# Optimization experiments

Hardware: AMD Instinct MI355X
Metric: run time of the kernel (lower is better)

## Reference

```python
import jax, jax.numpy as jnp
import numpy as np

B, N, C, H = 16, 4096, 384, 8
NH = N // H  # per-head patch chunk = 512


def setup_inputs() -> dict:
    key = jax.random.key(0)
    ks = jax.random.split(key, 5)
    s = 1.0 / np.sqrt(N)
    return {
        "x": jax.random.normal(ks[0], (B, N, C), dtype=jnp.float32),
        "wq": jax.random.normal(ks[1], (N, N), dtype=jnp.float32) * s,
        "wkv": jax.random.normal(ks[2], (2 * N, N), dtype=jnp.float32) * s,
        "wproj": jax.random.normal(ks[3], (N, N), dtype=jnp.float32) * s,
        "bproj": jax.random.normal(ks[4], (N,), dtype=jnp.float32) * s,
        "scale": jnp.ones((H, 1, 1), dtype=jnp.float32),
    }


def reference(x, wq, wkv, wproj, bproj, scale):
    # x: [B, N, C] -> token-mixing over patch dim N
    xt = jnp.swapaxes(x, -2, -1)                      # [B, C, N]
    q = jnp.einsum('bcn,mn->bcm', xt, wq)             # [B, C, N]
    kv = jnp.einsum('bcn,mn->bcm', xt, wkv)           # [B, C, 2N]
    q = q.reshape(B, C, H, NH).transpose(0, 2, 1, 3)  # [B, H, C, NH]
    kv = kv.reshape(B, C, 2, H, NH).transpose(2, 0, 3, 1, 4)  # [2, B, H, C, NH]
    k, v = kv[0], kv[1]
    q = q / jnp.linalg.norm(q, axis=-1, keepdims=True)
    k = k / jnp.linalg.norm(k, axis=-1, keepdims=True)
    # channel-reduction kernel trick: [B, H, 1, NH], scaled per head
    kernel_trick = (k * v).sum(axis=-2, keepdims=True) * scale
    o = q * kernel_trick                               # [B, H, C, NH]
    o = o.transpose(0, 2, 1, 3).reshape(B, C, N)       # [B, C, N]
    o = jax.nn.gelu(o, approximate=False)              # torch nn.GELU = exact erf
    o = jnp.einsum('bcn,mn->bcm', o, wproj) + bproj    # proj over patch dim
    return jnp.swapaxes(o, -2, -1)                     # [B, N, C]
```

## Files before the change

### kernel.cpp

```cpp
#include <hip/hip_runtime.h>
#include <hip/hip_bf16.h>
#include <math.h>
#include <stdint.h>

#define B_ 16
#define N_ 4096
#define C_ 384
#define H_ 8
#define NH_ 512

typedef __attribute__((ext_vector_type(8))) short short8;
typedef __attribute__((ext_vector_type(4))) float f32x4;

__device__ __forceinline__ unsigned short f2bf(float x) {
  uint32_t u = __builtin_bit_cast(uint32_t, x);
  uint32_t r = (u + 0x7fffu + ((u >> 16) & 1u)) >> 16;
  return (unsigned short)r;
}
__device__ __forceinline__ float bf2f(unsigned short u) {
  uint32_t v = ((uint32_t)u) << 16;
  return __builtin_bit_cast(float, v);
}

__device__ __forceinline__ void gl2lds16(const void* g, void* l) {
  __builtin_amdgcn_global_load_lds((__attribute__((address_space(1))) void*)g,
                                   (__attribute__((address_space(3))) void*)l,
                                   16, 0, 0);
}

__global__ void cvt_f32_bf16(const float* __restrict__ src,
                             unsigned short* __restrict__ dst, size_t n) {
  size_t i = ((size_t)blockIdx.x * blockDim.x + threadIdx.x) * 8;
  if (i >= n) return;
  float4 a = *(const float4*)(src + i);
  float4 b = *(const float4*)(src + i + 4);
  typedef __attribute__((ext_vector_type(8))) unsigned short u16x8;
  u16x8 o;
  o[0] = f2bf(a.x); o[1] = f2bf(a.y); o[2] = f2bf(a.z); o[3] = f2bf(a.w);
  o[4] = f2bf(b.x); o[5] = f2bf(b.y); o[6] = f2bf(b.z); o[7] = f2bf(b.w);
  *(u16x8*)(dst + i) = o;
}

__global__ __launch_bounds__(256)
void transpose_x(const float* __restrict__ x, unsigned short* __restrict__ xT) {
  __shared__ float tile[64 * 65];
  int b = blockIdx.z;
  int n0 = blockIdx.x * 64;
  int c0 = blockIdx.y * 64;
  int t = threadIdx.x;
  const float* xb = x + (size_t)b * N_ * C_;
  #pragma unroll
  for (int i = 0; i < 16; i++) {
    int r = i * 4 + (t >> 6);
    int cc = t & 63;
    tile[r * 65 + cc] = xb[(size_t)(n0 + r) * C_ + c0 + cc];
  }
  __syncthreads();
  unsigned short* xTb = xT + (size_t)b * C_ * N_;
  #pragma unroll
  for (int i = 0; i < 16; i++) {
    int r = i * 4 + (t >> 6);
    int nn = t & 63;
    xTb[(size_t)(c0 + r) * N_ + n0 + nn] = f2bf(tile[nn * 65 + r]);
  }
}

template <bool BIAS>
__global__ __launch_bounds__(256, 2)
void gemm_bt(const unsigned short* __restrict__ A,
             const unsigned short* __restrict__ Bt,
             void* __restrict__ OutV,
             const float* __restrict__ bias,
             size_t bStride, size_t outStride) {
  __shared__ unsigned short As[128 * 64];
  __shared__ unsigned short Bs[128 * 64];
  const int b  = blockIdx.x;
  const int m0 = blockIdx.y * 128;
  const int c0 = blockIdx.z * 128;
  const int t = threadIdx.x;
  const int lane = t & 63;
  const int w = t >> 6;
  const int wm = (w & 1) * 64;
  const int wn = (w >> 1) * 64;
  const int quad = lane >> 4;
  const int r16  = lane & 15;

  const unsigned short* Bb = Bt + (size_t)b * bStride;

  f32x4 acc[4][4];
  #pragma unroll
  for (int i = 0; i < 4; i++)
    #pragma unroll
    for (int j = 0; j < 4; j++)
      acc[i][j] = (f32x4){0.f, 0.f, 0.f, 0.f};

  const int rs = t >> 3;
  const int q8 = (t & 7) ^ (rs & 7);
  const unsigned short* aSrc = A  + (size_t)(m0 + rs) * 4096 + q8 * 8;
  const unsigned short* bSrc = Bb + (size_t)(c0 + rs) * 4096 + q8 * 8;
  unsigned short* aDst = As + t * 8;
  unsigned short* bDst = Bs + t * 8;

  for (int k0 = 0; k0 < 4096; k0 += 64) {
    #pragma unroll
    for (int p = 0; p < 4; p++) {
      gl2lds16(aSrc + (size_t)p * 32 * 4096 + k0, aDst + p * 2048);
      gl2lds16(bSrc + (size_t)p * 32 * 4096 + k0, bDst + p * 2048);
    }
    __syncthreads();
    #pragma unroll
    for (int kk = 0; kk < 2; kk++) {
      short8 af[4], bfv[4];
      const int cb = kk * 4 + quad;
      #pragma unroll
      for (int i = 0; i < 4; i++) {
        int ra = wm + i * 16 + r16;
        af[i]  = *(const short8*)(As + ra * 64 + ((cb ^ (ra & 7)) * 8));
        int rb = wn + i * 16 + r16;
        bfv[i] = *(const short8*)(Bs + rb * 64 + ((cb ^ (rb & 7)) * 8));
      }
      #pragma unroll
      for (int i = 0; i < 4; i++)
        #pragma unroll
        for (int j = 0; j < 4; j++)
          acc[i][j] = __builtin_amdgcn_mfma_f32_16x16x32_bf16(
              af[i], bfv[j], acc[i][j], 0, 0, 0);
    }
    __syncthreads();
  }

  if (BIAS) {
    float* Out = (float*)OutV + (size_t)b * outStride;
    #pragma unroll
    for (int i = 0; i < 4; i++) {
      #pragma unroll
      for (int v = 0; v < 4; v++) {
        int m = m0 + wm + i * 16 + quad * 4 + v;
        float bi = bias[m];
        #pragma unroll
        for (int j = 0; j < 4; j++) {
          int c = c0 + wn + j * 16 + r16;
          Out[(size_t)m * C_ + c] = acc[i][j][v] + bi;
        }
      }
    }
  } else {
    unsigned short* Out = (unsigned short*)OutV + (size_t)b * outStride;
    #pragma unroll
    for (int i = 0; i < 4; i++) {
      #pragma unroll
      for (int v = 0; v < 4; v++) {
        int m = m0 + wm + i * 16 + quad * 4 + v;
        #pragma unroll
        for (int j = 0; j < 4; j++) {
          int c = c0 + wn + j * 16 + r16;
          Out[(size_t)m * C_ + c] = f2bf(acc[i][j][v]);
        }
      }
    }
  }
}

__global__ __launch_bounds__(512)
void middle(const unsigned short* __restrict__ Y,
            unsigned short* __restrict__ GT,
            const float* __restrict__ scale) {
  const int h = blockIdx.x;
  const int b = blockIdx.y;
  const unsigned short* Yb = Y + (size_t)b * 12288 * C_;
  const unsigned short* Q = Yb + (size_t)(h * NH_) * C_;
  const unsigned short* K = Yb + (size_t)(N_ + h * NH_) * C_;
  const unsigned short* V = Yb + (size_t)(2 * N_ + h * NH_) * C_;
  unsigned short* GTb = GT + (size_t)b * C_ * N_ + h * NH_;

  __shared__ float invq[C_], invk[C_], kt[NH_];
  const int t = threadIdx.x;
  const float sc = scale[h];

  if (t < C_) {
    float sq = 0.f, sk = 0.f;
    for (int n = 0; n < NH_; n++) {
      float qv = bf2f(Q[(size_t)n * C_ + t]);
      float kv = bf2f(K[(size_t)n * C_ + t]);
      sq += qv * qv;
      sk += kv * kv;
    }
    invq[t] = rsqrtf(sq);
    invk[t] = rsqrtf(sk);
  }
  __syncthreads();

  {
    int w = t >> 6, l = t & 63;
    for (int n = w; n < NH_; n += 8) {
      float s = 0.f;
      for (int c = l; c < C_; c += 64)
        s += bf2f(K[(size_t)n * C_ + c]) * invk[c] * bf2f(V[(size_t)n * C_ + c]);
      #pragma unroll
      for (int o = 32; o > 0; o >>= 1) s += __shfl_xor(s, o);
      if (l == 0) kt[n] = s * sc;
    }
  }
  __syncthreads();

  {
    int n = t;
    float ktv = kt[n];
    for (int c = 0; c < C_; c++) {
      float xv = bf2f(Q[(size_t)n * C_ + c]) * invq[c] * ktv;
      float g = 0.5f * xv * (1.0f + erff(xv * 0.70710678118654752f));
      GTb[(size_t)c * N_ + n] = f2bf(g);
    }
  }
}

extern "C" void kernel_launch(void* const* d_in, const int* in_sizes, int n_in,
                              void* d_out, int out_size, void* d_ws, size_t ws_size,
                              hipStream_t stream) {
  const float* x     = (const float*)d_in[0];
  const float* wq    = (const float*)d_in[1];
  const float* wkv   = (const float*)d_in[2];
  const float* wproj = (const float*)d_in[3];
  const float* bproj = (const float*)d_in[4];
  const float* scale = (const float*)d_in[5];

  unsigned short* Wqkv = (unsigned short*)d_ws;
  unsigned short* Wp   = Wqkv + (size_t)12288 * 4096;
  unsigned short* xT   = Wp   + (size_t)4096 * 4096;
  unsigned short* Y    = xT   + (size_t)B_ * C_ * N_;
  unsigned short* GT   = Y    + (size_t)B_ * 12288 * C_;

  const size_t nq  = (size_t)4096 * 4096;
  const size_t nkv = (size_t)8192 * 4096;

  cvt_f32_bf16<<<(int)(nq  / 8 / 256), 256, 0, stream>>>(wq,    Wqkv,      nq);
  cvt_f32_bf16<<<(int)(nkv / 8 / 256), 256, 0, stream>>>(wkv,   Wqkv + nq, nkv);
  cvt_f32_bf16<<<(int)(nq  / 8 / 256), 256, 0, stream>>>(wproj, Wp,        nq);

  transpose_x<<<dim3(64, 6, 16), 256, 0, stream>>>(x, xT);

  gemm_bt<false><<<dim3(16, 96, 3), 256, 0, stream>>>(
      Wqkv, xT, Y, nullptr, (size_t)C_ * N_, (size_t)12288 * C_);

  middle<<<dim3(8, 16), 512, 0, stream>>>(Y, GT, scale);

  gemm_bt<true><<<dim3(16, 32, 3), 256, 0, stream>>>(
      Wp, GT, d_out, bproj, (size_t)C_ * N_, (size_t)N_ * C_);
}
```

Before: 1.391 ms.

## Replace QKV GEMM with batched 256x256 double-buffered pipelined MFMA kernel

Folds the batch dimension into the N dimension of the QKV projection so one large GEMM (12288 x 6144 x 4096) runs with 256x256 tiles, 8 waves, and double-buffered LDS fed by direct global-to-LDS loads. Loads are interleaved between MFMA phases using barriers, setprio and a block-index swizzle for L2 locality. This aims to raise data reuse and hide memory latency compared with the per-batch 128x128 kernel. The Y layout changes to [12288, B*C], so the middle kernel's indexing is updated. In exchange, LDS use and register pressure are higher, and the hand-tuned waitcnt schedule is fragile.

```diff
diff --git a/kernel.cpp b/kernel.cpp
--- a/kernel.cpp
+++ b/kernel.cpp
@@ -1,5 +1,4 @@
 #include <hip/hip_runtime.h>
-#include <hip/hip_bf16.h>
 #include <math.h>
 #include <stdint.h>
 
@@ -8,6 +7,7 @@
 #define C_ 384
 #define H_ 8
 #define NH_ 512
+#define NTOT_ 6144
 
 typedef __attribute__((ext_vector_type(8))) short short8;
 typedef __attribute__((ext_vector_type(4))) float f32x4;
@@ -26,6 +26,17 @@
   __builtin_amdgcn_global_load_lds((__attribute__((address_space(1))) void*)g,
                                    (__attribute__((address_space(3))) void*)l,
                                    16, 0, 0);
+}
+
+__device__ __forceinline__ void phase_mid() {
+  __builtin_amdgcn_s_barrier();
+  asm volatile("s_waitcnt lgkmcnt(0)" ::: "memory");
+  __builtin_amdgcn_sched_barrier(0);
+  __builtin_amdgcn_s_setprio(1);
+}
+__device__ __forceinline__ void phase_end() {
+  __builtin_amdgcn_s_setprio(0);
+  __builtin_amdgcn_s_barrier();
 }
 
 __global__ void cvt_f32_bf16(const float* __restrict__ src,
@@ -63,6 +74,133 @@
     int nn = t & 63;
     xTb[(size_t)(c0 + r) * N_ + n0 + nn] = f2bf(tile[nn * 65 + r]);
   }
+}
+
+__global__ __launch_bounds__(512, 2)
+void gemm256_bt(const unsigned short* __restrict__ A,
+                const unsigned short* __restrict__ Bt,
+                unsigned short* __restrict__ Out) {
+  __shared__ unsigned short As[2][2][128 * 64];
+  __shared__ unsigned short Bs[2][2][128 * 64];
+
+  const int bid = blockIdx.x;
+  const int swz = (bid & 7) * 144 + (bid >> 3);
+  const int mt = swz / 24, nt = swz % 24;
+  const int m0 = mt * 256, n0 = nt * 256;
+
+  const int t = threadIdx.x;
+  const int lane = t & 63;
+  const int w = t >> 6;
+  const int quad = lane >> 4;
+  const int r16 = lane & 15;
+  const int hA = w >> 2;
+  const int hB = (w >> 1) & 1;
+  const int rBb = (w & 1) * 64;
+  const int slot0 = quad ^ (r16 & 7);
+  const int slot1 = slot0 ^ 4;
+
+  f32x4 acc[8][4];
+  #pragma unroll
+  for (int i = 0; i < 8; i++)
+    #pragma unroll
+    for (int j = 0; j < 4; j++)
+      acc[i][j] = (f32x4){0.f, 0.f, 0.f, 0.f};
+
+  short8 af[4][2], bl[2][2], bh[2][2];
+
+  const int rs = t >> 3;
+  const int q8 = (t & 7) ^ (rs & 7);
+  const unsigned short* aS = A  + (size_t)(m0 + rs) * 4096 + q8 * 8;
+  const unsigned short* bS = Bt + (size_t)(n0 + rs) * 4096 + q8 * 8;
+
+  auto stA = [&](int d, int hf, int kt) {
+    const unsigned short* s =
+        aS + (size_t)hf * (128 * 4096) + (size_t)((kt & 63) * 64);
+    unsigned short* dp = &As[d][hf][t * 8];
+    gl2lds16(s, dp);
+    gl2lds16(s + (size_t)64 * 4096, dp + 4096);
+  };
+  auto stB = [&](int d, int hf, int kt) {
+    const unsigned short* s =
+        bS + (size_t)hf * (128 * 4096) + (size_t)((kt & 63) * 64);
+    unsigned short* dp = &Bs[d][hf][t * 8];
+    gl2lds16(s, dp);
+    gl2lds16(s + (size_t)64 * 4096, dp + 4096);
+  };
+  auto ldAh = [&](int d, int ih) {
+    #pragma unroll
+    for (int i = 0; i < 4; i++) {
+      const unsigned short* base = &As[d][hA][(ih * 64 + i * 16 + r16) * 64];
+      af[i][0] = *(const short8*)(base + slot0 * 8);
+      af[i][1] = *(const short8*)(base + slot1 * 8);
+    }
+  };
+  auto ldBh = [&](int d, int jh, short8 (&bfr)[2][2]) {
+    #pragma unroll
+    for (int j = 0; j < 2; j++) {
+      const unsigned short* base =
+          &Bs[d][hB][(rBb + jh * 32 + j * 16 + r16) * 64];
+      bfr[j][0] = *(const short8*)(base + slot0 * 8);
+      bfr[j][1] = *(const short8*)(base + slot1 * 8);
+    }
+  };
+  auto mfma16 = [&](int i0, int j0, short8 (&bfr)[2][2]) {
+    #pragma unroll
+    for (int i = 0; i < 4; i++)
+      #pragma unroll
+      for (int j = 0; j < 2; j++) {
+        acc[i0 + i][j0 + j] = __builtin_amdgcn_mfma_f32_16x16x32_bf16(
+            af[i][0], bfr[j][0], acc[i0 + i][j0 + j], 0, 0, 0);
+        acc[i0 + i][j0 + j] = __builtin_amdgcn_mfma_f32_16x16x32_bf16(
+            af[i][1], bfr[j][1], acc[i0 + i][j0 + j], 0, 0, 0);
+      }
+  };
+
+  stB(0, 0, 0); stB(0, 1, 0); stA(0, 0, 0); stA(0, 1, 0);
+  stB(1, 0, 1); stB(1, 1, 1);
+  asm volatile("s_waitcnt vmcnt(4)" ::: "memory");
+  __builtin_amdgcn_s_barrier();
+
+  for (int it = 0; it < 32; ++it) {
+    const int T = it * 2;
+    ldAh(0, 0); ldBh(0, 0, bl);
+    stA(1, 0, T + 1);
+    phase_mid(); mfma16(0, 0, bl); phase_end();
+    ldBh(0, 1, bh);
+    stA(1, 1, T + 1);
+    phase_mid(); mfma16(0, 2, bh); phase_end();
+    ldAh(0, 1);
+    stB(0, 0, T + 2);
+    phase_mid(); mfma16(4, 2, bh); phase_end();
+    stB(0, 1, T + 2);
+    asm volatile("s_waitcnt vmcnt(4)" ::: "memory");
+    phase_mid(); mfma16(4, 0, bl); phase_end();
+    ldAh(1, 0); ldBh(1, 0, bl);
+    stA(0, 0, T + 2);
+    phase_mid(); mfma16(0, 0, bl); phase_end();
+    ldBh(1, 1, bh);
+    stA(0, 1, T + 2);
+    phase_mid(); mfma16(0, 2, bh); phase_end();
+    ldAh(1, 1);
+    stB(1, 0, T + 3);
+    phase_mid(); mfma16(4, 2, bh); phase_end();
+    stB(1, 1, T + 3);
+    asm volatile("s_waitcnt vmcnt(4)" ::: "memory");
+    phase_mid(); mfma16(4, 0, bl); phase_end();
+  }
+
+  asm volatile("s_waitcnt vmcnt(0)" ::: "memory");
+
+  unsigned short* O = Out + (size_t)(m0 + hA * 128) * NTOT_ + n0 + (w & 3) * 64;
+  #pragma unroll
+  for (int i = 0; i < 8; i++)
+    #pragma unroll
+    for (int v = 0; v < 4; v++) {
+      const int m = i * 16 + quad * 4 + v;
+      #pragma unroll
+      for (int j = 0; j < 4; j++)
+        O[(size_t)m * NTOT_ + j * 16 + r16] = f2bf(acc[i][j][v]);
+    }
 }
 
 template <bool BIAS>
@@ -167,10 +305,9 @@
             const float* __restrict__ scale) {
   const int h = blockIdx.x;
   const int b = blockIdx.y;
-  const unsigned short* Yb = Y + (size_t)b * 12288 * C_;
-  const unsigned short* Q = Yb + (size_t)(h * NH_) * C_;
-  const unsigned short* K = Yb + (size_t)(N_ + h * NH_) * C_;
-  const unsigned short* V = Yb + (size_t)(2 * N_ + h * NH_) * C_;
+  const unsigned short* Q = Y + (size_t)(h * NH_) * NTOT_ + b * C_;
+  const unsigned short* K = Y + (size_t)(N_ + h * NH_) * NTOT_ + b * C_;
+  const unsigned short* V = Y + (size_t)(2 * N_ + h * NH_) * NTOT_ + b * C_;
   unsigned short* GTb = GT + (size_t)b * C_ * N_ + h * NH_;
 
   __shared__ float invq[C_], invk[C_], kt[NH_];
@@ -180,8 +317,8 @@
   if (t < C_) {
     float sq = 0.f, sk = 0.f;
     for (int n = 0; n < NH_; n++) {
-      float qv = bf2f(Q[(size_t)n * C_ + t]);
-      float kv = bf2f(K[(size_t)n * C_ + t]);
+      float qv = bf2f(Q[(size_t)n * NTOT_ + t]);
+      float kv = bf2f(K[(size_t)n * NTOT_ + t]);
       sq += qv * qv;
       sk += kv * kv;
     }
@@ -195,7 +332,8 @@
     for (int n = w; n < NH_; n += 8) {
       float s = 0.f;
       for (int c = l; c < C_; c += 64)
-        s += bf2f(K[(size_t)n * C_ + c]) * invk[c] * bf2f(V[(size_t)n * C_ + c]);
+        s += bf2f(K[(size_t)n * NTOT_ + c]) * invk[c] *
+             bf2f(V[(size_t)n * NTOT_ + c]);
       #pragma unroll
       for (int o = 32; o > 0; o >>= 1) s += __shfl_xor(s, o);
       if (l == 0) kt[n] = s * sc;
@@ -207,7 +345,7 @@
     int n = t;
     float ktv = kt[n];
     for (int c = 0; c < C_; c++) {
-      float xv = bf2f(Q[(size_t)n * C_ + c]) * invq[c] * ktv;
+      float xv = bf2f(Q[(size_t)n * NTOT_ + c]) * invq[c] * ktv;
       float g = 0.5f * xv * (1.0f + erff(xv * 0.70710678118654752f));
       GTb[(size_t)c * N_ + n] = f2bf(g);
     }
@@ -228,7 +366,7 @@
   unsigned short* Wp   = Wqkv + (size_t)12288 * 4096;
   unsigned short* xT   = Wp   + (size_t)4096 * 4096;
   unsigned short* Y    = xT   + (size_t)B_ * C_ * N_;
-  unsigned short* GT   = Y    + (size_t)B_ * 12288 * C_;
+  unsigned short* GT   = Y    + (size_t)12288 * NTOT_;
 
   const size_t nq  = (size_t)4096 * 4096;
   const size_t nkv = (size_t)8192 * 4096;
@@ -239,8 +377,7 @@
 
   transpose_x<<<dim3(64, 6, 16), 256, 0, stream>>>(x, xT);
 
-  gemm_bt<false><<<dim3(16, 96, 3), 256, 0, stream>>>(
-      Wqkv, xT, Y, nullptr, (size_t)C_ * N_, (size_t)12288 * C_);
+  gemm256_bt<<<dim3(48 * 24), 512, 0, stream>>>(Wqkv, xT, Y);
 
   middle<<<dim3(8, 16), 512, 0, stream>>>(Y, GT, scale);
 
```

Measured after the change: 1.411 ms. Within noise of the previous version (+1.4%).

## Split middle kernel into stats and apply kernels for more parallelism

Applied to the files above, without the earlier changes.

The single middle kernel, which had only 128 blocks, is split in two. A mid_stats kernel computes the inverse column norms of Q and K over 256 blocks and writes them into the dead Wqkv workspace. A mid_apply kernel then computes the kernel-trick vector and the GELU output over 256 blocks, each covering half the patch rows of a head, with threads also splitting the channel range. This gives more blocks to occupy the GPU's CUs and shortens each block's serial loop, at the cost of an extra launch and a global round trip for the norms.

```diff
diff --git a/kernel.cpp b/kernel.cpp
--- a/kernel.cpp
+++ b/kernel.cpp
@@ -1,5 +1,4 @@
 #include <hip/hip_runtime.h>
-#include <hip/hip_bf16.h>
 #include <math.h>
 #include <stdint.h>
 
@@ -161,53 +160,63 @@
   }
 }
 
+__global__ __launch_bounds__(384)
+void mid_stats(const unsigned short* __restrict__ Y,
+               float* __restrict__ invG) {
+  const int b = blockIdx.x, h = blockIdx.y, z = blockIdx.z;
+  const unsigned short* M =
+      Y + (size_t)b * 12288 * C_ + (size_t)(z * N_ + h * NH_) * C_;
+  const int c = threadIdx.x;
+  float s = 0.f;
+  for (int n = 0; n < NH_; n++) {
+    float v = bf2f(M[(size_t)n * C_ + c]);
+    s += v * v;
+  }
+  invG[((size_t)z * 128 + b * 8 + h) * C_ + c] = rsqrtf(s);
+}
+
 __global__ __launch_bounds__(512)
-void middle(const unsigned short* __restrict__ Y,
-            unsigned short* __restrict__ GT,
-            const float* __restrict__ scale) {
-  const int h = blockIdx.x;
-  const int b = blockIdx.y;
+void mid_apply(const unsigned short* __restrict__ Y,
+               unsigned short* __restrict__ GT,
+               const float* __restrict__ invG,
+               const float* __restrict__ scale) {
+  const int b = blockIdx.x, h = blockIdx.y, z = blockIdx.z;
   const unsigned short* Yb = Y + (size_t)b * 12288 * C_;
   const unsigned short* Q = Yb + (size_t)(h * NH_) * C_;
   const unsigned short* K = Yb + (size_t)(N_ + h * NH_) * C_;
   const unsigned short* V = Yb + (size_t)(2 * N_ + h * NH_) * C_;
+  const float* invQ = invG + ((size_t)b * 8 + h) * C_;
+  const float* invK = invG + ((size_t)128 + b * 8 + h) * C_;
   unsigned short* GTb = GT + (size_t)b * C_ * N_ + h * NH_;
 
-  __shared__ float invq[C_], invk[C_], kt[NH_];
+  __shared__ float kts[256];
   const int t = threadIdx.x;
   const float sc = scale[h];
-
-  if (t < C_) {
-    float sq = 0.f, sk = 0.f;
-    for (int n = 0; n < NH_; n++) {
-      float qv = bf2f(Q[(size_t)n * C_ + t]);
-      float kv = bf2f(K[(size_t)n * C_ + t]);
-      sq += qv * qv;
-      sk += kv * kv;
-    }
-    invq[t] = rsqrtf(sq);
-    invk[t] = rsqrtf(sk);
+  const int n0 = z * 256;
+
+  {
+    const int w = t >> 6, l = t & 63;
+    for (int i = 0; i < 32; i++) {
+      const int n = n0 + w * 32 + i;
+      float s = 0.f;
+      #pragma unroll
+      for (int ci = 0; ci < 6; ci++) {
+        const int c = l + ci * 64;
+        s += bf2f(K[(size_t)n * C_ + c]) * invK[c] * bf2f(V[(size_t)n * C_ + c]);
+      }
+      #pragma unroll
+      for (int o = 32; o > 0; o >>= 1) s += __shfl_xor(s, o);
+      if (l == 0) kts[n - n0] = s * sc;
+    }
   }
   __syncthreads();
 
   {
-    int w = t >> 6, l = t & 63;
-    for (int n = w; n < NH_; n += 8) {
-      float s = 0.f;
-      for (int c = l; c < C_; c += 64)
-        s += bf2f(K[(size_t)n * C_ + c]) * invk[c] * bf2f(V[(size_t)n * C_ + c]);
-      #pragma unroll
-      for (int o = 32; o > 0; o >>= 1) s += __shfl_xor(s, o);
-      if (l == 0) kt[n] = s * sc;
-    }
-  }
-  __syncthreads();
-
-  {
-    int n = t;
-    float ktv = kt[n];
-    for (int c = 0; c < C_; c++) {
-      float xv = bf2f(Q[(size_t)n * C_ + c]) * invq[c] * ktv;
+    const int n = n0 + (t & 255);
+    const int c0 = (t >> 8) * 192;
+    const float ktv = kts[n - n0];
+    for (int c = c0; c < c0 + 192; c++) {
+      float xv = bf2f(Q[(size_t)n * C_ + c]) * invQ[c] * ktv;
       float g = 0.5f * xv * (1.0f + erff(xv * 0.70710678118654752f));
       GTb[(size_t)c * N_ + n] = f2bf(g);
     }
@@ -229,6 +238,7 @@
   unsigned short* xT   = Wp   + (size_t)4096 * 4096;
   unsigned short* Y    = xT   + (size_t)B_ * C_ * N_;
   unsigned short* GT   = Y    + (size_t)B_ * 12288 * C_;
+  float* invG = (float*)Wqkv;
 
   const size_t nq  = (size_t)4096 * 4096;
   const size_t nkv = (size_t)8192 * 4096;
@@ -242,7 +252,8 @@
   gemm_bt<false><<<dim3(16, 96, 3), 256, 0, stream>>>(
       Wqkv, xT, Y, nullptr, (size_t)C_ * N_, (size_t)12288 * C_);
 
-  middle<<<dim3(8, 16), 512, 0, stream>>>(Y, GT, scale);
+  mid_stats<<<dim3(16, 8, 2), 384, 0, stream>>>(Y, invG);
+  mid_apply<<<dim3(16, 8, 2), 512, 0, stream>>>(Y, GT, invG, scale);
 
   gemm_bt<true><<<dim3(16, 32, 3), 256, 0, stream>>>(
       Wp, GT, d_out, bproj, (size_t)C_ * N_, (size_t)N_ * C_);
```

Result: faster. 1.206 ms (-13.3%).
